# Optimization experiments

Measured on AMD Instinct MI355X. Metric: run time of the kernel, lower is better.

## Reference

```python
import jax, jax.numpy as jnp
import numpy as np

NEG_SLOPE = 0.2

def setup_inputs() -> dict:
    key = jax.random.key(0)
    k1, k2, k3, k4, k5 = jax.random.split(key, 5)
    B, N, IN_DIM, H, D = 4, 2048, 256, 4, 64
    x = jax.random.normal(k1, (B, N, IN_DIM), dtype=jnp.float32)
    A_mask = jax.random.randint(k2, (N, N), 0, 2, dtype=jnp.int32)
    # xavier-like scaled params
    W = jax.random.normal(k3, (IN_DIM, H * D), dtype=jnp.float32) * (1.0 / np.sqrt(IN_DIM))
    a_src = jax.random.normal(k4, (H, D), dtype=jnp.float32) * (1.0 / np.sqrt(D))
    a_dst = jax.random.normal(k5, (H, D), dtype=jnp.float32) * (1.0 / np.sqrt(D))
    return {"x": x, "A_mask": A_mask, "W": W, "a_src": a_src, "a_dst": a_dst}

def reference(x, A_mask, W, a_src, a_dst):
    B, N, _ = x.shape
    H, D = a_src.shape
    # h: [B, N, H, D]
    h = (x @ W).reshape(B, N, H, D)
    # per-node attention scores: [B, N, H]
    src = jnp.einsum('bnhd,hd->bnh', h, a_src)
    dst = jnp.einsum('bnhd,hd->bnh', h, a_dst)
    # logits: [B, H, N, N] = src_i + dst_j, then leaky_relu
    logits = src.transpose(0, 2, 1)[:, :, :, None] + dst.transpose(0, 2, 1)[:, :, None, :]
    logits = jnp.where(logits >= 0, logits, NEG_SLOPE * logits)
    # mask (shared across batch and heads)
    logits = jnp.where(A_mask[None, None, :, :] == 0, -jnp.inf, logits)
    attn = jax.nn.softmax(logits, axis=-1)  # [B, H, N, N]
    # weighted sum over neighbors
    out = jnp.einsum('bhnm,bmhd->bnhd', attn, h).reshape(B, N, H * D)
    return jax.nn.elu(out)
```

## Files before the change

### kernel.cpp

```cpp
#include <hip/hip_runtime.h>

typedef float  f32x4 __attribute__((ext_vector_type(4)));
typedef short  s16x8 __attribute__((ext_vector_type(8)));

__device__ __forceinline__ unsigned short f2bf(float f){
    unsigned int u = __float_as_uint(f);
    u = u + 0x7FFFu + ((u >> 16) & 1u);
    return (unsigned short)(u >> 16);
}

__global__ void k_wt(const float* __restrict__ W, unsigned short* __restrict__ WT){
    int c = blockIdx.x, k = threadIdx.x;
    WT[c*256 + k] = f2bf(W[k*256 + c]);
}

__global__ void k_bits(const int* __restrict__ mask, unsigned long long* __restrict__ bits64){
    int i = blockIdx.x;
    int wave = threadIdx.x >> 6, lane = threadIdx.x & 63;
    for (int c = wave; c < 32; c += 4){
        int v = mask[i*2048 + c*64 + lane];
        unsigned long long b = __ballot(v != 0);
        if (lane == 0) bits64[i*32 + c] = b;
    }
}

__global__ __launch_bounds__(256) void k_gemm(const float* __restrict__ x,
        const unsigned short* __restrict__ WT,
        const float* __restrict__ a_src, const float* __restrict__ a_dst,
        unsigned short* __restrict__ hTt, float* __restrict__ src, float* __restrict__ dst){
    const int wave = threadIdx.x >> 6, lane = threadIdx.x & 63;
    const int q = lane >> 4, t = lane & 15;
    const int m0 = blockIdx.x*64 + wave*16;
    const int head = blockIdx.y;
    f32x4 acc[4] = {{0,0,0,0},{0,0,0,0},{0,0,0,0},{0,0,0,0}};
    const int row = m0 + t;
    for (int k = 0; k < 256; k += 32){
        int kk = k + q*8;
        const float* xp = x + row*256 + kk;
        f32x4 x0 = *reinterpret_cast<const f32x4*>(xp);
        f32x4 x1 = *reinterpret_cast<const f32x4*>(xp + 4);
        s16x8 a;
#pragma unroll
        for (int j = 0; j < 4; j++){ a[j] = (short)f2bf(x0[j]); a[j+4] = (short)f2bf(x1[j]); }
#pragma unroll
        for (int dblk = 0; dblk < 4; dblk++){
            s16x8 bfr = *reinterpret_cast<const s16x8*>(WT + (head*64 + dblk*16 + t)*256 + kk);
            acc[dblk] = __builtin_amdgcn_mfma_f32_16x16x32_bf16(a, bfr, acc[dblk], 0, 0, 0);
        }
    }
    const int b = m0 >> 11;
    const int bh = b*4 + head;
    const int jb = (m0 & 2047) >> 4;
    float as_[4], ad_[4];
#pragma unroll
    for (int dblk = 0; dblk < 4; dblk++){
        as_[dblk] = a_src[head*64 + dblk*16 + t];
        ad_[dblk] = a_dst[head*64 + dblk*16 + t];
    }
#pragma unroll
    for (int reg = 0; reg < 4; reg++){
        float sv = acc[0][reg]*as_[0] + acc[1][reg]*as_[1] + acc[2][reg]*as_[2] + acc[3][reg]*as_[3];
        float dv = acc[0][reg]*ad_[0] + acc[1][reg]*ad_[1] + acc[2][reg]*ad_[2] + acc[3][reg]*ad_[3];
#pragma unroll
        for (int off = 1; off < 16; off <<= 1){
            sv += __shfl_xor(sv, off);
            dv += __shfl_xor(dv, off);
        }
        if (t == 0){
            int n = (m0 + q*4 + reg) & 2047;
            src[bh*2048 + n] = sv;
            dst[bh*2048 + n] = dv;
        }
    }
#pragma unroll
    for (int dblk = 0; dblk < 4; dblk++){
        int d = dblk*16 + t;
#pragma unroll
        for (int reg = 0; reg < 4; reg++){
            int jj = q*4 + reg;
            hTt[((bh*128 + jb)*64 + d)*16 + jj] = f2bf(acc[dblk][reg]);
        }
    }
}

__global__ __launch_bounds__(256, 8) void k_attn(const unsigned short* __restrict__ hTt,
        const unsigned int* __restrict__ bits, const float* __restrict__ src,
        const float* __restrict__ dst, float* __restrict__ out){
    __shared__ float accL[4][16][64];
    __shared__ float Sl[4][16];
    const int bh = blockIdx.x;
    const int b = bh >> 2, head = bh & 3;
    const int wave = threadIdx.x >> 6, lane = threadIdx.x & 63;
    const int q = lane >> 4, t = lane & 15, q8 = q*8;
    const int i0 = blockIdx.y*16;
    const int i = i0 + t;
    const float NEGINF = -__builtin_inff();
    const float vsrc = src[bh*2048 + i];
    const unsigned int* bR = bits + i*64 + wave*16;
    const float* dR = dst + bh*2048 + wave*512 + q8;
    const unsigned short* vB = hTt + bh*131072 + wave*32768 + (q>>1)*1024 + (q&1)*8 + t*16;
    f32x4 acc0 = {0,0,0,0}, acc1 = {0,0,0,0}, acc2 = {0,0,0,0}, acc3 = {0,0,0,0};
    float S = 0.f;
    for (int it = 0; it < 16; ++it){
        const unsigned short* vp = vB + it*2048;
        s16x8 h0 = *reinterpret_cast<const s16x8*>(vp);
        s16x8 h1 = *reinterpret_cast<const s16x8*>(vp + 256);
        s16x8 h2 = *reinterpret_cast<const s16x8*>(vp + 512);
        s16x8 h3 = *reinterpret_cast<const s16x8*>(vp + 768);
        unsigned int bs = bR[it] >> q8;
        f32x4 d0 = *reinterpret_cast<const f32x4*>(dR + it*32);
        f32x4 d1 = *reinterpret_cast<const f32x4*>(dR + it*32 + 4);
        float e[8];
#pragma unroll
        for (int jj = 0; jj < 8; jj++){
            float dvv = (jj < 4) ? d0[jj] : d1[jj-4];
            float lg = vsrc + dvv;
            lg = fmaxf(lg, 0.2f*lg);
            lg = ((bs >> jj) & 1u) ? lg : NEGINF;
            e[jj] = __expf(lg);
        }
        union { unsigned int u[4]; s16x8 s; } pk;
#pragma unroll
        for (int p = 0; p < 4; p++)
            pk.u[p] = __builtin_amdgcn_perm(__float_as_uint(e[2*p+1]), __float_as_uint(e[2*p]), 0x07060302u);
        S += __uint_as_float(pk.u[0] << 16) + __uint_as_float(pk.u[0] & 0xFFFF0000u);
        S += __uint_as_float(pk.u[1] << 16) + __uint_as_float(pk.u[1] & 0xFFFF0000u);
        S += __uint_as_float(pk.u[2] << 16) + __uint_as_float(pk.u[2] & 0xFFFF0000u);
        S += __uint_as_float(pk.u[3] << 16) + __uint_as_float(pk.u[3] & 0xFFFF0000u);
        acc0 = __builtin_amdgcn_mfma_f32_16x16x32_bf16(pk.s, h0, acc0, 0,0,0);
        acc1 = __builtin_amdgcn_mfma_f32_16x16x32_bf16(pk.s, h1, acc1, 0,0,0);
        acc2 = __builtin_amdgcn_mfma_f32_16x16x32_bf16(pk.s, h2, acc2, 0,0,0);
        acc3 = __builtin_amdgcn_mfma_f32_16x16x32_bf16(pk.s, h3, acc3, 0,0,0);
    }
    S += __shfl_xor(S, 16);
    S += __shfl_xor(S, 32);
#pragma unroll
    for (int reg = 0; reg < 4; reg++){
        int r = q*4 + reg;
        accL[wave][r][ 0 + t] = acc0[reg];
        accL[wave][r][16 + t] = acc1[reg];
        accL[wave][r][32 + t] = acc2[reg];
        accL[wave][r][48 + t] = acc3[reg];
    }
    if (q == 0) Sl[wave][t] = S;
    __syncthreads();
    const int tid = threadIdx.x;
    const int row = tid >> 4;
    const int d   = (tid & 15) * 4;
    f32x4 v0 = *reinterpret_cast<const f32x4*>(&accL[0][row][d]);
    f32x4 v1 = *reinterpret_cast<const f32x4*>(&accL[1][row][d]);
    f32x4 v2 = *reinterpret_cast<const f32x4*>(&accL[2][row][d]);
    f32x4 v3 = *reinterpret_cast<const f32x4*>(&accL[3][row][d]);
    float Ssum = Sl[0][row] + Sl[1][row] + Sl[2][row] + Sl[3][row];
    float rS = 1.0f / Ssum;
    f32x4 v;
#pragma unroll
    for (int c = 0; c < 4; c++){
        float vv = (v0[c] + v1[c] + v2[c] + v3[c]) * rS;
        v[c] = vv > 0.f ? vv : (__expf(vv) - 1.0f);
    }
    *reinterpret_cast<f32x4*>(out + (b*2048 + i0 + row)*256 + head*64 + d) = v;
}

extern "C" void kernel_launch(void* const* d_in, const int* in_sizes, int n_in,
                              void* d_out, int out_size, void* d_ws, size_t ws_size,
                              hipStream_t stream) {
    const float* x     = (const float*)d_in[0];
    const int*   Amask = (const int*)d_in[1];
    const float* W     = (const float*)d_in[2];
    const float* a_src = (const float*)d_in[3];
    const float* a_dst = (const float*)d_in[4];
    float* out = (float*)d_out;

    char* ws = (char*)d_ws;
    unsigned short*     hTt  = (unsigned short*)(ws);
    unsigned long long* bits = (unsigned long long*)(ws + (4u<<20));
    unsigned short*     WT   = (unsigned short*)(ws + (4u<<20) + (512u<<10));
    float*              src  = (float*)(ws + (4u<<20) + (640u<<10));
    float*              dst  = (float*)(ws + (4u<<20) + (768u<<10));

    hipLaunchKernelGGL(k_wt,   dim3(256),      dim3(256), 0, stream, W, WT);
    hipLaunchKernelGGL(k_bits, dim3(2048),     dim3(256), 0, stream, Amask, bits);
    hipLaunchKernelGGL(k_gemm, dim3(128, 4),   dim3(256), 0, stream, x, WT, a_src, a_dst, hTt, src, dst);
    hipLaunchKernelGGL(k_attn, dim3(16, 128),  dim3(256), 0, stream, hTt, (const unsigned int*)bits, src, dst, out);
}
```

Measured before the change: 131.2 us.

## Process two 16-row tiles per attention block and compute row sums via MFMA

Each attention block now handles 32 query rows instead of 16, reusing each loaded tile of h and dst values for two sets of probabilities, which halves the global loads of h per output row. The softmax denominator is accumulated with an extra MFMA against a ones vector instead of scalar bf16 unpack-and-add per iteration. The cost is doubled accumulator registers, a lower occupancy hint (4 instead of 8 blocks), half as many blocks, and an extra barrier in the epilogue. The src/dst index expression in the GEMM epilogue is also rewritten equivalently.

```diff
diff --git a/kernel.cpp b/kernel.cpp
--- a/kernel.cpp
+++ b/kernel.cpp
@@ -67,7 +67,7 @@
             dv += __shfl_xor(dv, off);
         }
         if (t == 0){
-            int n = (m0 + q*4 + reg) & 2047;
+            int n = (m0 & 2047) + q*4 + reg;
             src[bh*2048 + n] = sv;
             dst[bh*2048 + n] = dv;
         }
@@ -83,7 +83,24 @@
     }
 }
 
-__global__ __launch_bounds__(256, 8) void k_attn(const unsigned short* __restrict__ hTt,
+__device__ __forceinline__ s16x8 make_p(unsigned int bs, float vsrc, f32x4 d0, f32x4 d1, float NEGINF){
+    float e[8];
+#pragma unroll
+    for (int jj = 0; jj < 8; jj++){
+        float dvv = (jj < 4) ? d0[jj] : d1[jj-4];
+        float lg = vsrc + dvv;
+        lg = fmaxf(lg, 0.2f*lg);
+        lg = ((bs >> jj) & 1u) ? lg : NEGINF;
+        e[jj] = __expf(lg);
+    }
+    union { unsigned int u[4]; s16x8 s; } pk;
+#pragma unroll
+    for (int p = 0; p < 4; p++)
+        pk.u[p] = __builtin_amdgcn_perm(__float_as_uint(e[2*p+1]), __float_as_uint(e[2*p]), 0x07060302u);
+    return pk.s;
+}
+
+__global__ __launch_bounds__(256, 4) void k_attn(const unsigned short* __restrict__ hTt,
         const unsigned int* __restrict__ bits, const float* __restrict__ src,
         const float* __restrict__ dst, float* __restrict__ out){
     __shared__ float accL[4][16][64];
@@ -92,74 +109,81 @@
     const int b = bh >> 2, head = bh & 3;
     const int wave = threadIdx.x >> 6, lane = threadIdx.x & 63;
     const int q = lane >> 4, t = lane & 15, q8 = q*8;
-    const int i0 = blockIdx.y*16;
-    const int i = i0 + t;
+    const int i0 = blockIdx.y*32;
     const float NEGINF = -__builtin_inff();
-    const float vsrc = src[bh*2048 + i];
-    const unsigned int* bR = bits + i*64 + wave*16;
+    const float vsrc0 = src[bh*2048 + i0 + t];
+    const float vsrc1 = src[bh*2048 + i0 + 16 + t];
+    const unsigned int* bR0 = bits + (i0 + t)*64 + wave*16;
+    const unsigned int* bR1 = bR0 + 16*64;
     const float* dR = dst + bh*2048 + wave*512 + q8;
     const unsigned short* vB = hTt + bh*131072 + wave*32768 + (q>>1)*1024 + (q&1)*8 + t*16;
-    f32x4 acc0 = {0,0,0,0}, acc1 = {0,0,0,0}, acc2 = {0,0,0,0}, acc3 = {0,0,0,0};
-    float S = 0.f;
+    f32x4 a00={0,0,0,0},a01={0,0,0,0},a02={0,0,0,0},a03={0,0,0,0};
+    f32x4 a10={0,0,0,0},a11={0,0,0,0},a12={0,0,0,0},a13={0,0,0,0};
+    f32x4 s0acc={0,0,0,0}, s1acc={0,0,0,0};
+    s16x8 ones;
+#pragma unroll
+    for (int j = 0; j < 8; j++) ones[j] = (short)0x3F80;
     for (int it = 0; it < 16; ++it){
         const unsigned short* vp = vB + it*2048;
         s16x8 h0 = *reinterpret_cast<const s16x8*>(vp);
         s16x8 h1 = *reinterpret_cast<const s16x8*>(vp + 256);
         s16x8 h2 = *reinterpret_cast<const s16x8*>(vp + 512);
         s16x8 h3 = *reinterpret_cast<const s16x8*>(vp + 768);
-        unsigned int bs = bR[it] >> q8;
+        unsigned int bs0 = bR0[it] >> q8;
+        unsigned int bs1 = bR1[it] >> q8;
         f32x4 d0 = *reinterpret_cast<const f32x4*>(dR + it*32);
         f32x4 d1 = *reinterpret_cast<const f32x4*>(dR + it*32 + 4);
-        float e[8];
-#pragma unroll
-        for (int jj = 0; jj < 8; jj++){
-            float dvv = (jj < 4) ? d0[jj] : d1[jj-4];
-            float lg = vsrc + dvv;
-            lg = fmaxf(lg, 0.2f*lg);
-            lg = ((bs >> jj) & 1u) ? lg : NEGINF;
-            e[jj] = __expf(lg);
-        }
-        union { unsigned int u[4]; s16x8 s; } pk;
-#pragma unroll
-        for (int p = 0; p < 4; p++)
-            pk.u[p] = __builtin_amdgcn_perm(__float_as_uint(e[2*p+1]), __float_as_uint(e[2*p]), 0x07060302u);
-        S += __uint_as_float(pk.u[0] << 16) + __uint_as_float(pk.u[0] & 0xFFFF0000u);
-        S += __uint_as_float(pk.u[1] << 16) + __uint_as_float(pk.u[1] & 0xFFFF0000u);
-        S += __uint_as_float(pk.u[2] << 16) + __uint_as_float(pk.u[2] & 0xFFFF0000u);
-        S += __uint_as_float(pk.u[3] << 16) + __uint_as_float(pk.u[3] & 0xFFFF0000u);
-        acc0 = __builtin_amdgcn_mfma_f32_16x16x32_bf16(pk.s, h0, acc0, 0,0,0);
-        acc1 = __builtin_amdgcn_mfma_f32_16x16x32_bf16(pk.s, h1, acc1, 0,0,0);
-        acc2 = __builtin_amdgcn_mfma_f32_16x16x32_bf16(pk.s, h2, acc2, 0,0,0);
-        acc3 = __builtin_amdgcn_mfma_f32_16x16x32_bf16(pk.s, h3, acc3, 0,0,0);
-    }
-    S += __shfl_xor(S, 16);
-    S += __shfl_xor(S, 32);
-#pragma unroll
-    for (int reg = 0; reg < 4; reg++){
-        int r = q*4 + reg;
-        accL[wave][r][ 0 + t] = acc0[reg];
-        accL[wave][r][16 + t] = acc1[reg];
-        accL[wave][r][32 + t] = acc2[reg];
-        accL[wave][r][48 + t] = acc3[reg];
-    }
-    if (q == 0) Sl[wave][t] = S;
-    __syncthreads();
-    const int tid = threadIdx.x;
-    const int row = tid >> 4;
-    const int d   = (tid & 15) * 4;
-    f32x4 v0 = *reinterpret_cast<const f32x4*>(&accL[0][row][d]);
-    f32x4 v1 = *reinterpret_cast<const f32x4*>(&accL[1][row][d]);
-    f32x4 v2 = *reinterpret_cast<const f32x4*>(&accL[2][row][d]);
-    f32x4 v3 = *reinterpret_cast<const f32x4*>(&accL[3][row][d]);
-    float Ssum = Sl[0][row] + Sl[1][row] + Sl[2][row] + Sl[3][row];
-    float rS = 1.0f / Ssum;
-    f32x4 v;
-#pragma unroll
-    for (int c = 0; c < 4; c++){
-        float vv = (v0[c] + v1[c] + v2[c] + v3[c]) * rS;
-        v[c] = vv > 0.f ? vv : (__expf(vv) - 1.0f);
-    }
-    *reinterpret_cast<f32x4*>(out + (b*2048 + i0 + row)*256 + head*64 + d) = v;
+        s16x8 p0 = make_p(bs0, vsrc0, d0, d1, NEGINF);
+        s16x8 p1 = make_p(bs1, vsrc1, d0, d1, NEGINF);
+        a00 = __builtin_amdgcn_mfma_f32_16x16x32_bf16(p0, h0, a00, 0,0,0);
+        a01 = __builtin_amdgcn_mfma_f32_16x16x32_bf16(p0, h1, a01, 0,0,0);
+        a02 = __builtin_amdgcn_mfma_f32_16x16x32_bf16(p0, h2, a02, 0,0,0);
+        a03 = __builtin_amdgcn_mfma_f32_16x16x32_bf16(p0, h3, a03, 0,0,0);
+        s0acc = __builtin_amdgcn_mfma_f32_16x16x32_bf16(p0, ones, s0acc, 0,0,0);
+        a10 = __builtin_amdgcn_mfma_f32_16x16x32_bf16(p1, h0, a10, 0,0,0);
+        a11 = __builtin_amdgcn_mfma_f32_16x16x32_bf16(p1, h1, a11, 0,0,0);
+        a12 = __builtin_amdgcn_mfma_f32_16x16x32_bf16(p1, h2, a12, 0,0,0);
+        a13 = __builtin_amdgcn_mfma_f32_16x16x32_bf16(p1, h3, a13, 0,0,0);
+        s1acc = __builtin_amdgcn_mfma_f32_16x16x32_bf16(p1, ones, s1acc, 0,0,0);
+    }
+#pragma unroll
+    for (int half = 0; half < 2; half++){
+        f32x4 c0 = half ? a10 : a00;
+        f32x4 c1 = half ? a11 : a01;
+        f32x4 c2 = half ? a12 : a02;
+        f32x4 c3 = half ? a13 : a03;
+        f32x4 sc = half ? s1acc : s0acc;
+        if (half) __syncthreads();
+#pragma unroll
+        for (int reg = 0; reg < 4; reg++){
+            int r = q*4 + reg;
+            accL[wave][r][ 0 + t] = c0[reg];
+            accL[wave][r][16 + t] = c1[reg];
+            accL[wave][r][32 + t] = c2[reg];
+            accL[wave][r][48 + t] = c3[reg];
+        }
+        if (t == 0){
+#pragma unroll
+            for (int reg = 0; reg < 4; reg++) Sl[wave][q*4 + reg] = sc[reg];
+        }
+        __syncthreads();
+        const int tid = threadIdx.x;
+        const int row = tid >> 4;
+        const int d   = (tid & 15) * 4;
+        f32x4 v0 = *reinterpret_cast<const f32x4*>(&accL[0][row][d]);
+        f32x4 v1 = *reinterpret_cast<const f32x4*>(&accL[1][row][d]);
+        f32x4 v2 = *reinterpret_cast<const f32x4*>(&accL[2][row][d]);
+        f32x4 v3 = *reinterpret_cast<const f32x4*>(&accL[3][row][d]);
+        float Ssum = Sl[0][row] + Sl[1][row] + Sl[2][row] + Sl[3][row];
+        float rS = 1.0f / Ssum;
+        f32x4 v;
+#pragma unroll
+        for (int c = 0; c < 4; c++){
+            float vv = (v0[c] + v1[c] + v2[c] + v3[c]) * rS;
+            v[c] = vv > 0.f ? vv : (__expf(vv) - 1.0f);
+        }
+        *reinterpret_cast<f32x4*>(out + (b*2048 + i0 + half*16 + row)*256 + head*64 + d) = v;
+    }
 }
 
 extern "C" void kernel_launch(void* const* d_in, const int* in_sizes, int n_in,
@@ -179,8 +203,8 @@
     float*              src  = (float*)(ws + (4u<<20) + (640u<<10));
     float*              dst  = (float*)(ws + (4u<<20) + (768u<<10));
 
-    hipLaunchKernelGGL(k_wt,   dim3(256),      dim3(256), 0, stream, W, WT);
-    hipLaunchKernelGGL(k_bits, dim3(2048),     dim3(256), 0, stream, Amask, bits);
-    hipLaunchKernelGGL(k_gemm, dim3(128, 4),   dim3(256), 0, stream, x, WT, a_src, a_dst, hTt, src, dst);
-    hipLaunchKernelGGL(k_attn, dim3(16, 128),  dim3(256), 0, stream, hTt, (const unsigned int*)bits, src, dst, out);
-}
+    hipLaunchKernelGGL(k_wt,   dim3(256),     dim3(256), 0, stream, W, WT);
+    hipLaunchKernelGGL(k_bits, dim3(2048),    dim3(256), 0, stream, Amask, bits);
+    hipLaunchKernelGGL(k_gemm, dim3(128, 4),  dim3(256), 0, stream, x, WT, a_src, a_dst, hTt, src, dst);
+    hipLaunchKernelGGL(k_attn, dim3(16, 64),  dim3(256), 0, stream, hTt, (const unsigned int*)bits, src, dst, out);
+}
```

Result: faster. 123.0 us (-6.2%).
